# Optimization experiments

Hardware: AMD Instinct MI355X
Metric: run time of the kernel (lower is better)

## Reference

```python
import jax, jax.numpy as jnp
import numpy as np

F, C, H, W = 16, 256, 64, 64
N, M = 4096, 8192


def setup_inputs() -> dict:
    key = jax.random.key(0)
    k1, k2, k3, k4, k5 = jax.random.split(key, 5)
    proj_mats = jax.random.normal(k1, (F, 3, 3), dtype=jnp.float32)
    feats = jax.random.normal(k2, (F, C, H, W), dtype=jnp.float32)
    feat_img = jax.random.randint(k3, (N, 1), 0, F, dtype=jnp.int32)
    feat_loc = jax.random.uniform(k4, (N, 2), dtype=jnp.float32) * 64.0
    # tracks: [2, M] matched feature pairs, smaller index first (code contract).
    pair = jax.random.randint(k5, (2, M), 0, N, dtype=jnp.int32)
    tracks = jnp.sort(pair, axis=0)
    return {"proj_mats": proj_mats, "feats": feats, "feat_img": feat_img,
            "feat_loc": feat_loc, "tracks": tracks, "n_img": F}


def _association(tracks, n, n_img):
    """Faithful translation of find_3d_point_association +
    associate_3d_point_indices_2_features. The torch code raises a sparse
    symmetric adjacency (with identity diagonal) to the n_img-th power and
    uses only its NONZERO PATTERN. We use binary exponentiation with
    saturation (min(.,1)), which preserves the nonzero pattern exactly
    (all values are non-negative) while keeping values bounded."""
    A = jnp.zeros((n, n), dtype=jnp.float32)
    A = A.at[tracks[0], tracks[1]].set(1.0)
    A = A.at[tracks[1], tracks[0]].set(1.0)
    d = jnp.arange(n)
    A = A.at[d, d].set(1.0)  # identity diagonal, as in the torch code

    # T = pattern(A ** n_img) via binary exponentiation (n_img is a Python int)
    R, P, e = None, A, int(n_img)
    while e:
        if e & 1:
            R = P if R is None else jnp.minimum(R @ P, 1.0)
        e >>= 1
        if e:
            P = jnp.minimum(P @ P, 1.0)
    T = R

    # leading[j] = min{ i : T[i,j] != 0, i <= j }  (diag guarantees j itself)
    rows = d[:, None]
    cand = jnp.where((T > 0) & (rows <= d[None, :]), rows, n)
    leading = cand.min(axis=0)  # [N] int32

    # self-leading features get consecutive 3D-point ids in index order;
    # everyone else inherits the id of its (self-leading) leading feature.
    is_self = leading == d
    point_id = jnp.cumsum(is_self.astype(jnp.int32)) - 1  # rank among self-leading
    association = point_id[leading]
    return association


def reference(proj_mats, feats, feat_img, feat_loc, tracks, n_img):
    n = feat_img.shape[0]
    association = _association(tracks, n, n_img)
    return association
```

## Files before the change

### kernel.cpp

```cpp
#include <hip/hip_runtime.h>

#define NTHREADS 1024
#define MAXN 4096
#define EPT 8
#define NWAVES (NTHREADS / 64)


__device__ __forceinline__ int find_halve(int* p, int x) {
    int px = p[x];
    while (px != x) {
        int gp = p[px];
        p[x] = gp;
        x = gp;
        px = p[x];
    }
    return x;
}

__device__ __forceinline__ int find_ro(const int* p, int x) {
    int px = p[x];
    while (px != x) { x = px; px = p[x]; }
    return x;
}

__global__ __launch_bounds__(NTHREADS) void ba_assoc_kernel(
    const int* __restrict__ tracks,
    int* __restrict__ out,
    int N, int M)
{
    const int tid  = threadIdx.x;
    const int lane = tid & 63;
    const int wid  = tid >> 6;

    __shared__ int par[MAXN];
    __shared__ int wsum[NWAVES];

    int eu[EPT], ev[EPT];
#pragma unroll
    for (int k = 0; k < EPT; ++k) {
        int e = tid + k * NTHREADS;
        if (e < M) { eu[k] = tracks[e]; ev[k] = tracks[M + e]; }
        else       { eu[k] = 0;         ev[k] = 0;             }
    }

    for (int i = tid; i < N; i += NTHREADS) par[i] = i;
    __syncthreads();

#pragma unroll
    for (int k = 0; k < EPT; ++k) {
        int u = eu[k], v = ev[k];
        while (true) {
            u = find_halve(par, u);
            v = find_halve(par, v);
            if (u == v) break;
            int lo = min(u, v), hi = max(u, v);
            if (atomicCAS(&par[hi], hi, lo) == hi) break;
            u = lo; v = hi;
        }
    }
    __syncthreads();

    const int base = tid * 4;
    int lead[4], f[4], s = 0;
#pragma unroll
    for (int k = 0; k < 4; ++k) {
        int idx = base + k;
        int r = (idx < N) ? find_ro(par, idx) : 0;
        lead[k] = r;
        int fl = (idx < N && r == idx) ? 1 : 0;
        f[k] = fl;
        s += fl;
    }

    int ps = s;
#pragma unroll
    for (int off = 1; off < 64; off <<= 1) {
        int t = __shfl_up(ps, off, 64);
        if (lane >= off) ps += t;
    }
    if (lane == 63) wsum[wid] = ps;
    __syncthreads();
    int wpre = 0;
    for (int w = 0; w < wid; ++w) wpre += wsum[w];
    int run = wpre + ps - s;

    __syncthreads();
#pragma unroll
    for (int k = 0; k < 4; ++k) {
        int idx = base + k;
        run += f[k];
        if (idx < N) par[idx] = run - 1;
    }
    __syncthreads();

#pragma unroll
    for (int k = 0; k < 4; ++k) {
        int idx = base + k;
        if (idx < N) out[idx] = par[lead[k]];
    }
}

extern "C" void kernel_launch(void* const* d_in, const int* in_sizes, int n_in,
                              void* d_out, int out_size, void* d_ws, size_t ws_size,
                              hipStream_t stream) {
    const int* tracks = (const int*)d_in[4];
    int* out = (int*)d_out;
    const int N = in_sizes[2];
    const int M = in_sizes[4] / 2;
    ba_assoc_kernel<<<1, NTHREADS, 0, stream>>>(tracks, out, N, M);
}
```

Measured before the change: 17.59 us.

## Replace CAS union-find with atomicMin hooking plus pointer-jumping passes

Replaces the find-with-path-halving plus atomicCAS union loop with an atomicMin-based union that walks parent pointers without first finding roots. It then adds two block-wide pointer-jumping passes to shorten parent chains before the read-only find. The aim is to cut the serialized find traversals and CAS retries during union. The trade-off is possibly longer chains that the later find_ro must walk, plus two extra __syncthreads barriers.

Result: faster. 17.06 us (-3.0%).

```diff
diff --git a/kernel.cpp b/kernel.cpp
--- a/kernel.cpp
+++ b/kernel.cpp
@@ -6,15 +6,13 @@
 #define NWAVES (NTHREADS / 64)
 
 
-__device__ __forceinline__ int find_halve(int* p, int x) {
-    int px = p[x];
-    while (px != x) {
-        int gp = p[px];
-        p[x] = gp;
-        x = gp;
-        px = p[x];
+__device__ __forceinline__ void unite_min(int* p, int u, int v) {
+    while (u != v) {
+        if (u > v) { int t = u; u = v; v = t; }
+        int old = atomicMin(&p[v], u);
+        if (old == v) return;
+        v = old;
     }
-    return x;
 }
 
 __device__ __forceinline__ int find_ro(const int* p, int x) {
@@ -47,20 +45,24 @@
     __syncthreads();
 
 #pragma unroll
-    for (int k = 0; k < EPT; ++k) {
-        int u = eu[k], v = ev[k];
-        while (true) {
-            u = find_halve(par, u);
-            v = find_halve(par, v);
-            if (u == v) break;
-            int lo = min(u, v), hi = max(u, v);
-            if (atomicCAS(&par[hi], hi, lo) == hi) break;
-            u = lo; v = hi;
-        }
-    }
+    for (int k = 0; k < EPT; ++k) unite_min(par, eu[k], ev[k]);
     __syncthreads();
 
     const int base = tid * 4;
+#pragma unroll
+    for (int r = 0; r < 2; ++r) {
+#pragma unroll
+        for (int k = 0; k < 4; ++k) {
+            int idx = base + k;
+            if (idx < N) {
+                int p1 = par[idx];
+                int p2 = par[p1];
+                if (p2 < p1) par[idx] = p2;
+            }
+        }
+        __syncthreads();
+    }
+
     int lead[4], f[4], s = 0;
 #pragma unroll
     for (int k = 0; k < 4; ++k) {
```
